# Optimization experiments

Measured on AMD Instinct MI355X. Metric: run time of the kernel, lower is better.

## Reference

```python
import jax, jax.numpy as jnp
import numpy as np

S = 10        # spiking_segment_count
TEMP = 50.0

def setup_inputs() -> dict:
    key = jax.random.key(0)
    ks = jax.random.split(key, 6)
    bs, din, dout = 2048, 1024, 1024
    x = jax.random.normal(ks[0], (bs, din), dtype=jnp.float32)
    t = jax.random.uniform(ks[1], (bs,), dtype=jnp.float32)  # in [0,1) subset of [-1,1]
    scale = 1.0 / np.sqrt(din)
    param_W = jax.random.normal(ks[2], (din, dout * S * 3), dtype=jnp.float32) * scale
    param_b = jax.random.normal(ks[3], (dout * S * 3,), dtype=jnp.float32) * 0.01
    norm_W = jax.random.normal(ks[4], (din, dout), dtype=jnp.float32) * scale
    norm_b = jax.random.normal(ks[5], (dout,), dtype=jnp.float32) * 0.01
    return {"x": x, "t": t, "param_W": param_W, "param_b": param_b,
            "norm_W": norm_W, "norm_b": norm_b}

def reference(x, t, param_W, param_b, norm_W, norm_b):
    bs = x.shape[0]
    dout = norm_W.shape[1]
    # param GEMM -> (bs, S, dout, 3)
    params = (x @ param_W + param_b).reshape(bs, S, dout, 3)
    weights = jax.nn.softmax(params[..., 0], axis=1)                 # (bs, S, dout)
    keypoints = jnp.concatenate(
        [jnp.zeros_like(weights[:, :1]), jnp.cumsum(weights, axis=1)], axis=1
    ) * 2.0 - 1.0                                                    # (bs, S+1, dout)
    slopes = jnp.tanh(params[..., 1])
    intercepts = params[..., 2]
    tt = t.reshape(-1, 1, 1)                                         # (bs, 1, 1)
    starts = keypoints[:, :S]
    ends = keypoints[:, 1:]
    residual = slopes * tt + intercepts                              # (bs, S, dout)
    validity = ((tt >= starts) & (tt < ends)) | ((tt == 1.0) & (ends == 1.0))
    vf = validity.astype(x.dtype)
    left_margin = jnp.sum((tt - starts) * vf, axis=1)                # (bs, dout)
    right_margin = jnp.sum((ends - tt) * vf, axis=1)
    lw = jax.nn.sigmoid(-TEMP * left_margin)
    rw = jax.nn.sigmoid(-TEMP * right_margin)
    lv = jnp.concatenate([vf[:, :1], vf[:, :-1]], axis=1)
    rv = jnp.concatenate([vf[:, 1:], vf[:, -1:]], axis=1)
    sw = -(lw + rw - 1.0)
    result = (lw * jnp.sum(residual * lv, axis=1)
              + sw * jnp.sum(residual * vf, axis=1)
              + rw * jnp.sum(residual * rv, axis=1))
    # norm == 'constant': subtract segment-wise integral, add norm_net(x)
    integral = jnp.sum(0.5 * slopes * (ends * ends - starts * starts)
                       + intercepts * weights, axis=1) * 0.5
    norm_target = x @ norm_W + norm_b
    return result - integral + norm_target
```

## Files before the change

kernel.cpp:

```cpp
#include <hip/hip_runtime.h>
#include <cstdint>
#include <cstddef>

#define BS    2048
#define DIN   1024
#define DOUT  1024
#define SSEG  10
#define NPAR  30720
#define NPK   20480
#define NCOL2 21504
#define NLG   10240
#define NT_LG 80
#define NT_SM 168
#define TAU   5e-5f
#define WL_CAP 1048576u

typedef _Float16 half_t;
typedef __attribute__((ext_vector_type(8))) _Float16 half8;
typedef __attribute__((ext_vector_type(4))) _Float16 half4;
typedef __attribute__((ext_vector_type(2))) _Float16 half2v;
typedef __attribute__((ext_vector_type(4))) float   floatx4;

__device__ __forceinline__ void gload16(const void* g, void* l) {
  __builtin_amdgcn_global_load_lds(
      (const __attribute__((address_space(1))) void*)g,
      (__attribute__((address_space(3))) void*)l, 16, 0, 0);
}

__global__ void k_zero(unsigned* c) { if (threadIdx.x == 0) *c = 0; }

__global__ __launch_bounds__(256) void k_split_x(const float* __restrict__ x,
                                                 half_t* __restrict__ xh,
                                                 half_t* __restrict__ xl,
                                                 unsigned* __restrict__ cnt) {
  if (blockIdx.x == 0 && threadIdx.x == 0) *cnt = 0;
  int i = blockIdx.x * 256 + threadIdx.x;
  floatx4 v = ((const floatx4*)x)[i];
  half4 h, l;
  #pragma unroll
  for (int c = 0; c < 4; c++) { h[c] = (half_t)v[c]; l[c] = (half_t)(v[c] - (float)h[c]); }
  ((half4*)xh)[i] = h;
  ((half4*)xl)[i] = l;
}

__global__ __launch_bounds__(256) void k_transw(const float* __restrict__ src,
                                                half_t* __restrict__ wsm,
                                                half_t* __restrict__ wh,
                                                half_t* __restrict__ wlo,
                                                float* __restrict__ wlt) {
  __shared__ float tile[32][384];
  int bx = blockIdx.x;
  int k0 = blockIdx.y * 32;
  int tid = threadIdx.x;
  int s  = bx >> 3;
  int d0 = (bx & 7) * 128;
  const float* sb = src + (size_t)k0 * NPAR + bx * 384;
  for (int i = tid; i < 32 * 96; i += 256) {
    int r = i / 96, q = i - r * 96;
    ((floatx4*)&tile[r][0])[q] = ((const floatx4*)(sb + (size_t)r * NPAR))[q];
  }
  __syncthreads();
  int j   = tid & 127;
  int ks  = (tid >> 7) * 16;
  {
    size_t row = (size_t)(s * 1024 + d0 + j) * DIN + k0 + ks;
    #pragma unroll
    for (int m = 0; m < 16; m++) {
      float raw = tile[ks + m][3 * j];
      float v = raw * 32.0f;
      half_t h = (half_t)v;
      wlt[row + m] = raw;
      wh [row + m] = h;
      wlo[row + m] = (half_t)(v - (float)h);
    }
  }
  #pragma unroll
  for (int c = 0; c < 2; c++) {
    size_t row = (size_t)(s * 2048 + 2 * (d0 + j) + c) * DIN + k0 + ks;
    #pragma unroll
    for (int m = 0; m < 16; m++)
      wsm[row + m] = (half_t)tile[ks + m][3 * j + 1 + c];
  }
}

__global__ __launch_bounds__(256) void k_transpose(const float* __restrict__ src,
                                                   half_t* __restrict__ dst,
                                                   int ncols, int col_off) {
  __shared__ float tile[32][33];
  int tx = threadIdx.x & 31;
  int ty = threadIdx.x >> 5;
  int col0 = blockIdx.x * 32;
  int k0   = blockIdx.y * 32;
  #pragma unroll
  for (int r = ty; r < 32; r += 8)
    tile[r][tx] = src[(size_t)(k0 + r) * ncols + col0 + tx];
  __syncthreads();
  #pragma unroll
  for (int r = ty; r < 32; r += 8)
    dst[(size_t)(col0 + r + col_off) * DIN + k0 + tx] = (half_t)tile[tx][r];
}

__global__ __launch_bounds__(256) void k_gemm_all(const half_t* __restrict__ Ah,
                                                  const half_t* __restrict__ Al,
                                                  const half_t* __restrict__ Wsm,
                                                  const half_t* __restrict__ Bh,
                                                  const half_t* __restrict__ Bl,
                                                  half_t* __restrict__ P,
                                                  float* __restrict__ Lg,
                                                  const float* __restrict__ pb,
                                                  const float* __restrict__ nb) {
  __shared__ __attribute__((aligned(16))) half_t s0[128 * 32];
  __shared__ __attribute__((aligned(16))) half_t s1[128 * 32];
  __shared__ __attribute__((aligned(16))) half_t s2[128 * 32];
  __shared__ __attribute__((aligned(16))) half_t s3[128 * 32];
  const int K = DIN;
  int bx = blockIdx.x;
  int m0 = blockIdx.y * 128;
  int tid = threadIdx.x, w = tid >> 6, L = tid & 63;
  int wm = (w >> 1) * 64, wn = (w & 1) * 64;
  int l15 = L & 15, quad = L >> 4;

  size_t arow = (size_t)(m0 + w * 16 + (L >> 2)) * K + (L & 3) * 8;
  char* l0 = (char*)s0 + w * 1024;
  char* l1 = (char*)s1 + w * 1024;
  char* l2 = (char*)s2 + w * 1024;
  char* l3 = (char*)s3 + w * 1024;

  floatx4 acc[4][4] = {};

  if (bx < NT_LG) {
    int n0 = bx * 128;
    size_t brow = (size_t)(n0 + w * 16 + (L >> 2)) * K + (L & 3) * 8;

    for (int k0 = 0; k0 < K; k0 += 32) {
      __syncthreads();
      gload16(Ah + arow + k0,          l0);
      gload16(Ah + arow + 64 * K + k0, l0 + 4096);
      gload16(Al + arow + k0,          l1);
      gload16(Al + arow + 64 * K + k0, l1 + 4096);
      gload16(Bh + brow + k0,          l2);
      gload16(Bh + brow + 64 * K + k0, l2 + 4096);
      gload16(Bl + brow + k0,          l3);
      gload16(Bl + brow + 64 * K + k0, l3 + 4096);
      __syncthreads();

      #pragma unroll
      for (int mi = 0; mi < 4; mi++) {
        half8 afh = *(const half8*)((const char*)s0 + (wm + mi * 16 + l15) * 64 + quad * 16);
        half8 afl = *(const half8*)((const char*)s1 + (wm + mi * 16 + l15) * 64 + quad * 16);
        #pragma unroll
        for (int ni = 0; ni < 4; ni++) {
          half8 bfh = *(const half8*)((const char*)s2 + (wn + ni * 16 + l15) * 64 + quad * 16);
          half8 bfl = *(const half8*)((const char*)s3 + (wn + ni * 16 + l15) * 64 + quad * 16);
          floatx4 a = acc[mi][ni];
          a = __builtin_amdgcn_mfma_f32_16x16x32_f16(afh, bfh, a, 0, 0, 0);
          a = __builtin_amdgcn_mfma_f32_16x16x32_f16(afl, bfh, a, 0, 0, 0);
          a = __builtin_amdgcn_mfma_f32_16x16x32_f16(afh, bfl, a, 0, 0, 0);
          acc[mi][ni] = a;
        }
      }
    }

    #pragma unroll
    for (int ni = 0; ni < 4; ni++) {
      int col = n0 + wn + ni * 16 + l15;
      float bias = pb[(col >> 10) * 3072 + (col & 1023) * 3];
      #pragma unroll
      for (int mi = 0; mi < 4; mi++) {
        int row = m0 + wm + mi * 16 + quad * 4;
        floatx4 v = acc[mi][ni];
        #pragma unroll
        for (int r = 0; r < 4; r++)
          Lg[(size_t)(row + r) * NLG + col] = v[r] * 0.03125f + bias;
      }
    }
  } else {
    int n0 = (bx - NT_LG) * 128;
    size_t brow = (size_t)(n0 + w * 16 + (L >> 2)) * K + (L & 3) * 8;

    for (int k0 = 0; k0 < K; k0 += 32) {
      __syncthreads();
      gload16(Ah + arow + k0,           l0);
      gload16(Ah + arow + 64 * K + k0,  l0 + 4096);
      gload16(Wsm + brow + k0,          l2);
      gload16(Wsm + brow + 64 * K + k0, l2 + 4096);
      __syncthreads();

      half8 af[4], bf[4];
      #pragma unroll
      for (int mi = 0; mi < 4; mi++)
        af[mi] = *(const half8*)((const char*)s0 + (wm + mi * 16 + l15) * 64 + quad * 16);
      #pragma unroll
      for (int ni = 0; ni < 4; ni++)
        bf[ni] = *(const half8*)((const char*)s2 + (wn + ni * 16 + l15) * 64 + quad * 16);
      #pragma unroll
      for (int mi = 0; mi < 4; mi++)
        #pragma unroll
        for (int ni = 0; ni < 4; ni++)
          acc[mi][ni] = __builtin_amdgcn_mfma_f32_16x16x32_f16(af[mi], bf[ni], acc[mi][ni], 0, 0, 0);
    }

    #pragma unroll
    for (int ni = 0; ni < 4; ni++) {
      int col = n0 + wn + ni * 16 + l15;
      float bias;
      if (col < NPK) {
        int s = col >> 11, rem = col & 2047;
        bias = pb[s * 3072 + 3 * (rem >> 1) + 1 + (rem & 1)];
      } else {
        bias = nb[col - NPK];
      }
      #pragma unroll
      for (int mi = 0; mi < 4; mi++) {
        int row = m0 + wm + mi * 16 + quad * 4;
        floatx4 v = acc[mi][ni];
        #pragma unroll
        for (int r = 0; r < 4; r++)
          P[(size_t)(row + r) * NCOL2 + col] = (half_t)(v[r] + bias);
      }
    }
  }
}

__device__ __forceinline__ float spiking_eval(const float* p, float tt, float* mind) {
  float mx = -1e30f;
  #pragma unroll
  for (int s = 0; s < SSEG; s++) mx = fmaxf(mx, p[3 * s]);
  float ew[10], wsum = 0.0f;
  #pragma unroll
  for (int s = 0; s < SSEG; s++) { ew[s] = __expf(p[3 * s] - mx); wsum += ew[s]; }
  float inv = 1.0f / wsum;

  float kp[11];
  kp[0] = -1.0f;
  float cum = 0.0f, md = 1e30f;
  #pragma unroll
  for (int s = 0; s < SSEG; s++) {
    cum += ew[s] * inv;
    kp[s + 1] = cum * 2.0f - 1.0f;
    md = fminf(md, fabsf(tt - kp[s + 1]));
  }
  *mind = md;

  float vf[10], resid[10];
  float lm = 0.0f, rm = 0.0f, integ = 0.0f;
  #pragma unroll
  for (int s = 0; s < SSEG; s++) {
    float p1 = p[3 * s + 1], p2 = p[3 * s + 2];
    float e2 = __expf(2.0f * fabsf(p1));
    float th = copysignf(1.0f - 2.0f / (e2 + 1.0f), p1);
    resid[s] = th * tt + p2;
    float st = kp[s], en = kp[s + 1];
    bool v = ((tt >= st) && (tt < en)) || ((tt == 1.0f) && (en == 1.0f));
    float vv = v ? 1.0f : 0.0f;
    vf[s] = vv;
    lm += (tt - st) * vv;
    rm += (en - tt) * vv;
    integ += 0.5f * th * (en * en - st * st) + p2 * (ew[s] * inv);
  }
  float resLV = 0.0f, resV = 0.0f, resRV = 0.0f;
  #pragma unroll
  for (int s = 0; s < SSEG; s++) {
    float lv = (s == 0) ? vf[0] : vf[s - 1];
    float rv = (s == 9) ? vf[9] : vf[s + 1];
    resLV += resid[s] * lv;
    resV  += resid[s] * vf[s];
    resRV += resid[s] * rv;
  }
  float lw = 1.0f / (1.0f + __expf(50.0f * lm));
  float rw = 1.0f / (1.0f + __expf(50.0f * rm));
  float swt = 1.0f - lw - rw;
  return lw * resLV + swt * resV + rw * resRV - 0.5f * integ + p[30];
}

__global__ __launch_bounds__(256) void k_pointwise(const half_t* __restrict__ P,
                                                   const float* __restrict__ Lg,
                                                   const float* __restrict__ t,
                                                   float* __restrict__ out,
                                                   unsigned* __restrict__ cnt,
                                                   unsigned* __restrict__ wl,
                                                   unsigned cap) {
  __shared__ __attribute__((aligned(16))) half_t sp[SSEG * 512];
  int b = blockIdx.x, dg = blockIdx.y, tid = threadIdx.x;
  const half_t* Pb = P + (size_t)b * NCOL2;
  for (int i = tid; i < SSEG * 64; i += 256) {
    int s = i >> 6, e = i & 63;
    ((uint4*)sp)[(s << 6) + e] = ((const uint4*)(Pb + s * 2048 + dg * 512))[e];
  }
  float tt = t[b];
  float nt = (float)Pb[NPK + dg * 256 + tid];
  const float* Lb = Lg + (size_t)b * NLG + dg * 256 + tid;
  __syncthreads();

  float p[31];
  #pragma unroll
  for (int s = 0; s < SSEG; s++) {
    p[3 * s] = Lb[s * 1024];
    half2v hv = ((const half2v*)sp)[s * 256 + tid];
    p[3 * s + 1] = (float)hv.x;
    p[3 * s + 2] = (float)hv.y;
  }
  p[30] = nt;
  float mind;
  float r = spiking_eval(p, tt, &mind);
  int d = dg * 256 + tid;
  out[(size_t)b * DOUT + d] = r;
  if (wl != nullptr && mind < TAU) {
    unsigned idx = atomicAdd(cnt, 1u);
    if (idx < cap) wl[idx] = ((unsigned)b << 10) | (unsigned)d;
  }
}

__global__ __launch_bounds__(256) void k_naive(const float* __restrict__ x,
                                               const float* __restrict__ t,
                                               const float* __restrict__ pW,
                                               const float* __restrict__ pb,
                                               const float* __restrict__ nW,
                                               const float* __restrict__ nb,
                                               float* __restrict__ out,
                                               unsigned* __restrict__ cnt,
                                               unsigned* __restrict__ wl,
                                               unsigned cap) {
  __shared__ float xs[DIN];
  int b = blockIdx.x, dg = blockIdx.y, tid = threadIdx.x;
  for (int i = tid; i < DIN; i += 256) xs[i] = x[(size_t)b * DIN + i];
  __syncthreads();
  int d = dg * 256 + tid;
  float acc[31];
  #pragma unroll
  for (int i = 0; i < 31; i++) acc[i] = 0.0f;
  for (int k = 0; k < DIN; k++) {
    float xv = xs[k];
    const float* wr = pW + (size_t)k * NPAR + 3 * d;
    #pragma unroll
    for (int s = 0; s < SSEG; s++) {
      acc[3 * s]     += xv * wr[s * 3072];
      acc[3 * s + 1] += xv * wr[s * 3072 + 1];
      acc[3 * s + 2] += xv * wr[s * 3072 + 2];
    }
    acc[30] += xv * nW[(size_t)k * DOUT + d];
  }
  #pragma unroll
  for (int s = 0; s < SSEG; s++) {
    acc[3 * s]     += pb[s * 3072 + 3 * d];
    acc[3 * s + 1] += pb[s * 3072 + 3 * d + 1];
    acc[3 * s + 2] += pb[s * 3072 + 3 * d + 2];
  }
  acc[30] += nb[d];
  float mind;
  float r = spiking_eval(acc, t[b], &mind);
  out[(size_t)b * DOUT + d] = r;
  if (wl != nullptr && mind < TAU) {
    unsigned idx = atomicAdd(cnt, 1u);
    if (idx < cap) wl[idx] = ((unsigned)b << 10) | (unsigned)d;
  }
}

__global__ __launch_bounds__(256) void k_redo(const float* __restrict__ x,
                                              const float* __restrict__ t,
                                              const float* __restrict__ pW,
                                              const float* __restrict__ pb,
                                              const float* __restrict__ nW,
                                              const float* __restrict__ nb,
                                              const half_t* __restrict__ P,
                                              const float* __restrict__ WLt,
                                              int haveP,
                                              const unsigned* __restrict__ cnt,
                                              const unsigned* __restrict__ wl,
                                              unsigned cap,
                                              float* __restrict__ out) {
  unsigned n = *cnt;
  if (n > cap) n = cap;
  int lane = threadIdx.x & 63;
  unsigned wave = (blockIdx.x * 256 + threadIdx.x) >> 6;
  unsigned nwaves = (gridDim.x * 256) >> 6;

  for (unsigned e = wave; e < n; e += nwaves) {
    unsigned code = wl[e];
    int b = (int)(code >> 10), d = (int)(code & 1023);

    double lg[10], sl[10], ic[10], nt = 0.0;
    #pragma unroll
    for (int s = 0; s < SSEG; s++) { lg[s] = 0.0; sl[s] = 0.0; ic[s] = 0.0; }

    if (haveP) {
      for (int k = lane; k < DIN; k += 64) {
        double xv = (double)x[(size_t)b * DIN + k];
        #pragma unroll
        for (int s = 0; s < SSEG; s++)
          lg[s] += xv * (double)WLt[(size_t)(s * 1024 + d) * DIN + k];
      }
    } else {
      for (int k = lane; k < DIN; k += 64) {
        double xv = (double)x[(size_t)b * DIN + k];
        const float* wr = pW + (size_t)k * NPAR + 3 * d;
        #pragma unroll
        for (int s = 0; s < SSEG; s++) {
          lg[s] += xv * (double)wr[s * 3072];
          sl[s] += xv * (double)wr[s * 3072 + 1];
          ic[s] += xv * (double)wr[s * 3072 + 2];
        }
        nt += xv * (double)nW[(size_t)k * DOUT + d];
      }
    }
    #pragma unroll
    for (int off = 32; off > 0; off >>= 1) {
      #pragma unroll
      for (int s = 0; s < SSEG; s++) lg[s] += __shfl_down(lg[s], off);
      if (!haveP) {
        #pragma unroll
        for (int s = 0; s < SSEG; s++) {
          sl[s] += __shfl_down(sl[s], off);
          ic[s] += __shfl_down(ic[s], off);
        }
        nt += __shfl_down(nt, off);
      }
    }

    if (lane == 0) {
      double slope[10], icpt[10], ntv;
      if (haveP) {
        const half_t* Pr = P + (size_t)b * NCOL2;
        #pragma unroll
        for (int s = 0; s < SSEG; s++) {
          slope[s] = tanh((double)(float)Pr[s * 2048 + 2 * d]);
          icpt[s]  = (double)(float)Pr[s * 2048 + 2 * d + 1];
        }
        ntv = (double)(float)Pr[NPK + d];
      } else {
        #pragma unroll
        for (int s = 0; s < SSEG; s++) {
          slope[s] = tanh(sl[s] + (double)pb[s * 3072 + 3 * d + 1]);
          icpt[s]  = ic[s] + (double)pb[s * 3072 + 3 * d + 2];
        }
        ntv = nt + (double)nb[d];
      }
      #pragma unroll
      for (int s = 0; s < SSEG; s++) lg[s] += (double)pb[s * 3072 + 3 * d];

      double mx = -1e300;
      #pragma unroll
      for (int s = 0; s < SSEG; s++) mx = fmax(mx, lg[s]);
      double ew[10], ws = 0.0;
      #pragma unroll
      for (int s = 0; s < SSEG; s++) { ew[s] = exp(lg[s] - mx); ws += ew[s]; }

      double kp[11];
      kp[0] = -1.0;
      double cum = 0.0;
      #pragma unroll
      for (int s = 0; s < SSEG; s++) { cum += ew[s] / ws; kp[s + 1] = cum * 2.0 - 1.0; }

      double tt = (double)t[b];
      double vf[10], resid[10], lm = 0.0, rm = 0.0, integ = 0.0;
      #pragma unroll
      for (int s = 0; s < SSEG; s++) {
        double st = kp[s], en = kp[s + 1];
        bool v = ((tt >= st) && (tt < en)) || ((tt == 1.0) && (en == 1.0));
        double vv = v ? 1.0 : 0.0;
        vf[s] = vv;
        resid[s] = slope[s] * tt + icpt[s];
        lm += (tt - st) * vv;
        rm += (en - tt) * vv;
        integ += 0.5 * slope[s] * (en * en - st * st) + icpt[s] * (ew[s] / ws);
      }
      double rLV = 0.0, rV = 0.0, rRV = 0.0;
      #pragma unroll
      for (int s = 0; s < SSEG; s++) {
        double lv = (s == 0) ? vf[0] : vf[s - 1];
        double rv = (s == 9) ? vf[9] : vf[s + 1];
        rLV += resid[s] * lv;
        rV  += resid[s] * vf[s];
        rRV += resid[s] * rv;
      }
      double lw = 1.0 / (1.0 + exp(50.0 * lm));
      double rw = 1.0 / (1.0 + exp(50.0 * rm));
      double res = lw * rLV + (1.0 - lw - rw) * rV + rw * rRV - 0.5 * integ + ntv;
      out[(size_t)b * DOUT + d] = (float)res;
    }
  }
}

extern "C" void kernel_launch(void* const* d_in, const int* in_sizes, int n_in,
                              void* d_out, int out_size, void* d_ws, size_t ws_size,
                              hipStream_t stream) {
  const float* x  = (const float*)d_in[0];
  const float* t  = (const float*)d_in[1];
  const float* pW = (const float*)d_in[2];
  const float* pb = (const float*)d_in[3];
  const float* nW = (const float*)d_in[4];
  const float* nb = (const float*)d_in[5];
  float* out = (float*)d_out;

  const size_t o_cnt = 0;
  const size_t o_wl  = 64;
  const size_t o_xh  = o_wl  + (size_t)WL_CAP * 4;
  const size_t o_xl  = o_xh  + (size_t)BS * DIN * 2;
  const size_t o_wsm = o_xl  + (size_t)BS * DIN * 2;
  const size_t o_wh  = o_wsm + (size_t)NCOL2 * DIN * 2;
  const size_t o_wlo = o_wh  + (size_t)NLG * DIN * 2;
  const size_t o_wlt = o_wlo + (size_t)NLG * DIN * 2;
  const size_t o_p   = o_wlt + (size_t)NLG * DIN * 4;
  const size_t o_lg  = o_p   + (size_t)BS * NCOL2 * 2;
  const size_t need  = o_lg  + (size_t)BS * NLG * 4;

  bool have_wl = ws_size >= 1024 * 1024;
  unsigned* cnt = (unsigned*)((char*)d_ws + o_cnt);
  unsigned* wl  = (unsigned*)((char*)d_ws + o_wl);
  unsigned cap  = 0;
  if (have_wl) {
    size_t avail = (ws_size >= need) ? (size_t)WL_CAP
                                     : (ws_size - o_wl) / 4;
    cap = (unsigned)(avail < WL_CAP ? avail : WL_CAP);
  }

  if (ws_size >= need) {
    half_t* xh  = (half_t*)((char*)d_ws + o_xh);
    half_t* xl  = (half_t*)((char*)d_ws + o_xl);
    half_t* wsm = (half_t*)((char*)d_ws + o_wsm);
    half_t* wh  = (half_t*)((char*)d_ws + o_wh);
    half_t* wlo = (half_t*)((char*)d_ws + o_wlo);
    float*  wlt = (float*)((char*)d_ws + o_wlt);
    half_t* P   = (half_t*)((char*)d_ws + o_p);
    float*  Lg  = (float*)((char*)d_ws + o_lg);

    k_split_x<<<(BS * DIN) / 1024, 256, 0, stream>>>(x, xh, xl, cnt);
    k_transw<<<dim3(NPAR / 384, DIN / 32), 256, 0, stream>>>(pW, wsm, wh, wlo, wlt);
    k_transpose<<<dim3(DOUT / 32, DIN / 32), 256, 0, stream>>>(nW, wsm, DOUT, NPK);
    k_gemm_all<<<dim3(NT_LG + NT_SM, BS / 128), 256, 0, stream>>>(xh, xl, wsm, wh, wlo,
                                                                  P, Lg, pb, nb);
    k_pointwise<<<dim3(BS, DOUT / 256), 256, 0, stream>>>(P, Lg, t, out, cnt,
                                                          have_wl ? wl : nullptr, cap);
    if (have_wl)
      k_redo<<<256, 256, 0, stream>>>(x, t, pW, pb, nW, nb, P, wlt, 1, cnt, wl, cap, out);
  } else {
    if (have_wl) k_zero<<<1, 64, 0, stream>>>(cnt);
    k_naive<<<dim3(BS, DOUT / 256), 256, 0, stream>>>(x, t, pW, pb, nW, nb, out, cnt,
                                                      have_wl ? wl : nullptr, cap);
    if (have_wl)
      k_redo<<<256, 256, 0, stream>>>(x, t, pW, pb, nW, nb, nullptr, nullptr, 0,
                                      cnt, wl, cap, out);
  }
}
```

Baseline: 629.9 us.

## Split fused GEMM into two kernels with swizzled tile order, merge prep kernels

Splits the combined GEMM into a 3-MFMA split-precision logit kernel and a single-precision kernel, so each kernel uses only the LDS it needs (raising occupancy for the lighter one) and avoids branch divergence across blocks. Adds a grouped block-index swizzle in which 8 consecutive blocks share one M tile and cover 8 N tiles, aimed at better L2 reuse of weight tiles. Folds the norm-weight transpose into the x-split kernel to save a launch. The cost is one extra GEMM launch and the loss of overlap between the heavy and light tile types within a single grid.

```diff
diff --git a/kernel.cpp b/kernel.cpp
--- a/kernel.cpp
+++ b/kernel.cpp
@@ -12,6 +12,7 @@
 #define NLG   10240
 #define NT_LG 80
 #define NT_SM 168
+#define MT    16
 #define TAU   5e-5f
 #define WL_CAP 1048576u
 
@@ -29,18 +30,37 @@
 
 __global__ void k_zero(unsigned* c) { if (threadIdx.x == 0) *c = 0; }
 
-__global__ __launch_bounds__(256) void k_split_x(const float* __restrict__ x,
-                                                 half_t* __restrict__ xh,
-                                                 half_t* __restrict__ xl,
-                                                 unsigned* __restrict__ cnt) {
-  if (blockIdx.x == 0 && threadIdx.x == 0) *cnt = 0;
-  int i = blockIdx.x * 256 + threadIdx.x;
-  floatx4 v = ((const floatx4*)x)[i];
-  half4 h, l;
-  #pragma unroll
-  for (int c = 0; c < 4; c++) { h[c] = (half_t)v[c]; l[c] = (half_t)(v[c] - (float)h[c]); }
-  ((half4*)xh)[i] = h;
-  ((half4*)xl)[i] = l;
+__global__ __launch_bounds__(256) void k_prep(const float* __restrict__ x,
+                                              half_t* __restrict__ xh,
+                                              half_t* __restrict__ xl,
+                                              const float* __restrict__ nW,
+                                              half_t* __restrict__ wsm,
+                                              unsigned* __restrict__ cnt) {
+  int bid = blockIdx.x;
+  if (bid < 2048) {
+    if (bid == 0 && threadIdx.x == 0) *cnt = 0;
+    int i = bid * 256 + threadIdx.x;
+    floatx4 v = ((const floatx4*)x)[i];
+    half4 h, l;
+    #pragma unroll
+    for (int c = 0; c < 4; c++) { h[c] = (half_t)v[c]; l[c] = (half_t)(v[c] - (float)h[c]); }
+    ((half4*)xh)[i] = h;
+    ((half4*)xl)[i] = l;
+  } else {
+    __shared__ float tile[32][33];
+    int b2 = bid - 2048;
+    int col0 = (b2 & 31) * 32;
+    int k0   = (b2 >> 5) * 32;
+    int tx = threadIdx.x & 31;
+    int ty = threadIdx.x >> 5;
+    #pragma unroll
+    for (int r = ty; r < 32; r += 8)
+      tile[r][tx] = nW[(size_t)(k0 + r) * DOUT + col0 + tx];
+    __syncthreads();
+    #pragma unroll
+    for (int r = ty; r < 32; r += 8)
+      wsm[(size_t)(col0 + r + NPK) * DIN + k0 + tx] = (half_t)tile[tx][r];
+  }
 }
 
 __global__ __launch_bounds__(256) void k_transw(const float* __restrict__ src,
@@ -83,141 +103,145 @@
   }
 }
 
-__global__ __launch_bounds__(256) void k_transpose(const float* __restrict__ src,
-                                                   half_t* __restrict__ dst,
-                                                   int ncols, int col_off) {
-  __shared__ float tile[32][33];
-  int tx = threadIdx.x & 31;
-  int ty = threadIdx.x >> 5;
-  int col0 = blockIdx.x * 32;
-  int k0   = blockIdx.y * 32;
-  #pragma unroll
-  for (int r = ty; r < 32; r += 8)
-    tile[r][tx] = src[(size_t)(k0 + r) * ncols + col0 + tx];
-  __syncthreads();
-  #pragma unroll
-  for (int r = ty; r < 32; r += 8)
-    dst[(size_t)(col0 + r + col_off) * DIN + k0 + tx] = (half_t)tile[tx][r];
-}
-
-__global__ __launch_bounds__(256) void k_gemm_all(const half_t* __restrict__ Ah,
-                                                  const half_t* __restrict__ Al,
-                                                  const half_t* __restrict__ Wsm,
-                                                  const half_t* __restrict__ Bh,
-                                                  const half_t* __restrict__ Bl,
-                                                  half_t* __restrict__ P,
-                                                  float* __restrict__ Lg,
-                                                  const float* __restrict__ pb,
-                                                  const float* __restrict__ nb) {
-  __shared__ __attribute__((aligned(16))) half_t s0[128 * 32];
-  __shared__ __attribute__((aligned(16))) half_t s1[128 * 32];
-  __shared__ __attribute__((aligned(16))) half_t s2[128 * 32];
-  __shared__ __attribute__((aligned(16))) half_t s3[128 * 32];
+__device__ __forceinline__ void swizzle_mn(int bid, int* mt, int* nt) {
+  int x = bid & 7;
+  int g = bid >> 3;
+  *mt = g & 15;
+  *nt = (g >> 4) * 8 + x;
+}
+
+__global__ __launch_bounds__(256) void k_gemm_logit(const half_t* __restrict__ Ah,
+                                                    const half_t* __restrict__ Al,
+                                                    const half_t* __restrict__ Bh,
+                                                    const half_t* __restrict__ Bl,
+                                                    float* __restrict__ Lg,
+                                                    const float* __restrict__ pb) {
+  __shared__ __attribute__((aligned(16))) half_t sAh[128 * 32];
+  __shared__ __attribute__((aligned(16))) half_t sAl[128 * 32];
+  __shared__ __attribute__((aligned(16))) half_t sBh[128 * 32];
+  __shared__ __attribute__((aligned(16))) half_t sBl[128 * 32];
   const int K = DIN;
-  int bx = blockIdx.x;
-  int m0 = blockIdx.y * 128;
+  int mt, nt;
+  swizzle_mn(blockIdx.x, &mt, &nt);
+  int m0 = mt * 128, n0 = nt * 128;
   int tid = threadIdx.x, w = tid >> 6, L = tid & 63;
   int wm = (w >> 1) * 64, wn = (w & 1) * 64;
   int l15 = L & 15, quad = L >> 4;
 
   size_t arow = (size_t)(m0 + w * 16 + (L >> 2)) * K + (L & 3) * 8;
-  char* l0 = (char*)s0 + w * 1024;
-  char* l1 = (char*)s1 + w * 1024;
-  char* l2 = (char*)s2 + w * 1024;
-  char* l3 = (char*)s3 + w * 1024;
+  size_t brow = (size_t)(n0 + w * 16 + (L >> 2)) * K + (L & 3) * 8;
+  char* lah = (char*)sAh + w * 1024;
+  char* lal = (char*)sAl + w * 1024;
+  char* lbh = (char*)sBh + w * 1024;
+  char* lbl = (char*)sBl + w * 1024;
 
   floatx4 acc[4][4] = {};
 
-  if (bx < NT_LG) {
-    int n0 = bx * 128;
-    size_t brow = (size_t)(n0 + w * 16 + (L >> 2)) * K + (L & 3) * 8;
-
-    for (int k0 = 0; k0 < K; k0 += 32) {
-      __syncthreads();
-      gload16(Ah + arow + k0,          l0);
-      gload16(Ah + arow + 64 * K + k0, l0 + 4096);
-      gload16(Al + arow + k0,          l1);
-      gload16(Al + arow + 64 * K + k0, l1 + 4096);
-      gload16(Bh + brow + k0,          l2);
-      gload16(Bh + brow + 64 * K + k0, l2 + 4096);
-      gload16(Bl + brow + k0,          l3);
-      gload16(Bl + brow + 64 * K + k0, l3 + 4096);
-      __syncthreads();
-
-      #pragma unroll
-      for (int mi = 0; mi < 4; mi++) {
-        half8 afh = *(const half8*)((const char*)s0 + (wm + mi * 16 + l15) * 64 + quad * 16);
-        half8 afl = *(const half8*)((const char*)s1 + (wm + mi * 16 + l15) * 64 + quad * 16);
-        #pragma unroll
-        for (int ni = 0; ni < 4; ni++) {
-          half8 bfh = *(const half8*)((const char*)s2 + (wn + ni * 16 + l15) * 64 + quad * 16);
-          half8 bfl = *(const half8*)((const char*)s3 + (wn + ni * 16 + l15) * 64 + quad * 16);
-          floatx4 a = acc[mi][ni];
-          a = __builtin_amdgcn_mfma_f32_16x16x32_f16(afh, bfh, a, 0, 0, 0);
-          a = __builtin_amdgcn_mfma_f32_16x16x32_f16(afl, bfh, a, 0, 0, 0);
-          a = __builtin_amdgcn_mfma_f32_16x16x32_f16(afh, bfl, a, 0, 0, 0);
-          acc[mi][ni] = a;
-        }
-      }
-    }
-
-    #pragma unroll
-    for (int ni = 0; ni < 4; ni++) {
-      int col = n0 + wn + ni * 16 + l15;
-      float bias = pb[(col >> 10) * 3072 + (col & 1023) * 3];
-      #pragma unroll
-      for (int mi = 0; mi < 4; mi++) {
-        int row = m0 + wm + mi * 16 + quad * 4;
-        floatx4 v = acc[mi][ni];
-        #pragma unroll
-        for (int r = 0; r < 4; r++)
-          Lg[(size_t)(row + r) * NLG + col] = v[r] * 0.03125f + bias;
-      }
-    }
-  } else {
-    int n0 = (bx - NT_LG) * 128;
-    size_t brow = (size_t)(n0 + w * 16 + (L >> 2)) * K + (L & 3) * 8;
-
-    for (int k0 = 0; k0 < K; k0 += 32) {
-      __syncthreads();
-      gload16(Ah + arow + k0,           l0);
-      gload16(Ah + arow + 64 * K + k0,  l0 + 4096);
-      gload16(Wsm + brow + k0,          l2);
-      gload16(Wsm + brow + 64 * K + k0, l2 + 4096);
-      __syncthreads();
-
-      half8 af[4], bf[4];
-      #pragma unroll
-      for (int mi = 0; mi < 4; mi++)
-        af[mi] = *(const half8*)((const char*)s0 + (wm + mi * 16 + l15) * 64 + quad * 16);
+  for (int k0 = 0; k0 < K; k0 += 32) {
+    __syncthreads();
+    gload16(Ah + arow + k0,          lah);
+    gload16(Ah + arow + 64 * K + k0, lah + 4096);
+    gload16(Al + arow + k0,          lal);
+    gload16(Al + arow + 64 * K + k0, lal + 4096);
+    gload16(Bh + brow + k0,          lbh);
+    gload16(Bh + brow + 64 * K + k0, lbh + 4096);
+    gload16(Bl + brow + k0,          lbl);
+    gload16(Bl + brow + 64 * K + k0, lbl + 4096);
+    __syncthreads();
+
+    #pragma unroll
+    for (int mi = 0; mi < 4; mi++) {
+      half8 afh = *(const half8*)((const char*)sAh + (wm + mi * 16 + l15) * 64 + quad * 16);
+      half8 afl = *(const half8*)((const char*)sAl + (wm + mi * 16 + l15) * 64 + quad * 16);
+      #pragma unroll
+      for (int ni = 0; ni < 4; ni++) {
+        half8 bfh = *(const half8*)((const char*)sBh + (wn + ni * 16 + l15) * 64 + quad * 16);
+        half8 bfl = *(const half8*)((const char*)sBl + (wn + ni * 16 + l15) * 64 + quad * 16);
+        floatx4 a = acc[mi][ni];
+        a = __builtin_amdgcn_mfma_f32_16x16x32_f16(afh, bfh, a, 0, 0, 0);
+        a = __builtin_amdgcn_mfma_f32_16x16x32_f16(afl, bfh, a, 0, 0, 0);
+        a = __builtin_amdgcn_mfma_f32_16x16x32_f16(afh, bfl, a, 0, 0, 0);
+        acc[mi][ni] = a;
+      }
+    }
+  }
+
+  #pragma unroll
+  for (int ni = 0; ni < 4; ni++) {
+    int col = n0 + wn + ni * 16 + l15;
+    float bias = pb[(col >> 10) * 3072 + (col & 1023) * 3];
+    #pragma unroll
+    for (int mi = 0; mi < 4; mi++) {
+      int row = m0 + wm + mi * 16 + quad * 4;
+      floatx4 v = acc[mi][ni];
+      #pragma unroll
+      for (int r = 0; r < 4; r++)
+        Lg[(size_t)(row + r) * NLG + col] = v[r] * 0.03125f + bias;
+    }
+  }
+}
+
+__global__ __launch_bounds__(256) void k_gemm_sm(const half_t* __restrict__ A,
+                                                 const half_t* __restrict__ B,
+                                                 half_t* __restrict__ P,
+                                                 const float* __restrict__ pb,
+                                                 const float* __restrict__ nb) {
+  __shared__ __attribute__((aligned(16))) half_t As[128 * 32];
+  __shared__ __attribute__((aligned(16))) half_t Bs[128 * 32];
+  const int K = DIN;
+  int mt, nt;
+  swizzle_mn(blockIdx.x, &mt, &nt);
+  int m0 = mt * 128, n0 = nt * 128;
+  int tid = threadIdx.x, w = tid >> 6, L = tid & 63;
+  int wm = (w >> 1) * 64, wn = (w & 1) * 64;
+  int l15 = L & 15, quad = L >> 4;
+
+  const half_t* ga = A + (size_t)(m0 + w * 16 + (L >> 2)) * K + (L & 3) * 8;
+  const half_t* gb = B + (size_t)(n0 + w * 16 + (L >> 2)) * K + (L & 3) * 8;
+  char* lA = (char*)As + w * 1024;
+  char* lB = (char*)Bs + w * 1024;
+
+  floatx4 acc[4][4] = {};
+
+  for (int k0 = 0; k0 < K; k0 += 32) {
+    __syncthreads();
+    gload16(ga + k0,          lA);
+    gload16(ga + 64 * K + k0, lA + 4096);
+    gload16(gb + k0,          lB);
+    gload16(gb + 64 * K + k0, lB + 4096);
+    __syncthreads();
+
+    half8 af[4], bf[4];
+    #pragma unroll
+    for (int mi = 0; mi < 4; mi++)
+      af[mi] = *(const half8*)((const char*)As + (wm + mi * 16 + l15) * 64 + quad * 16);
+    #pragma unroll
+    for (int ni = 0; ni < 4; ni++)
+      bf[ni] = *(const half8*)((const char*)Bs + (wn + ni * 16 + l15) * 64 + quad * 16);
+    #pragma unroll
+    for (int mi = 0; mi < 4; mi++)
       #pragma unroll
       for (int ni = 0; ni < 4; ni++)
-        bf[ni] = *(const half8*)((const char*)s2 + (wn + ni * 16 + l15) * 64 + quad * 16);
-      #pragma unroll
-      for (int mi = 0; mi < 4; mi++)
-        #pragma unroll
-        for (int ni = 0; ni < 4; ni++)
-          acc[mi][ni] = __builtin_amdgcn_mfma_f32_16x16x32_f16(af[mi], bf[ni], acc[mi][ni], 0, 0, 0);
-    }
-
-    #pragma unroll
-    for (int ni = 0; ni < 4; ni++) {
-      int col = n0 + wn + ni * 16 + l15;
-      float bias;
-      if (col < NPK) {
-        int s = col >> 11, rem = col & 2047;
-        bias = pb[s * 3072 + 3 * (rem >> 1) + 1 + (rem & 1)];
-      } else {
-        bias = nb[col - NPK];
-      }
-      #pragma unroll
-      for (int mi = 0; mi < 4; mi++) {
-        int row = m0 + wm + mi * 16 + quad * 4;
-        floatx4 v = acc[mi][ni];
-        #pragma unroll
-        for (int r = 0; r < 4; r++)
-          P[(size_t)(row + r) * NCOL2 + col] = (half_t)(v[r] + bias);
-      }
+        acc[mi][ni] = __builtin_amdgcn_mfma_f32_16x16x32_f16(af[mi], bf[ni], acc[mi][ni], 0, 0, 0);
+  }
+
+  #pragma unroll
+  for (int ni = 0; ni < 4; ni++) {
+    int col = n0 + wn + ni * 16 + l15;
+    float bias;
+    if (col < NPK) {
+      int s = col >> 11, rem = col & 2047;
+      bias = pb[s * 3072 + 3 * (rem >> 1) + 1 + (rem & 1)];
+    } else {
+      bias = nb[col - NPK];
+    }
+    #pragma unroll
+    for (int mi = 0; mi < 4; mi++) {
+      int row = m0 + wm + mi * 16 + quad * 4;
+      floatx4 v = acc[mi][ni];
+      #pragma unroll
+      for (int r = 0; r < 4; r++)
+        P[(size_t)(row + r) * NCOL2 + col] = (half_t)(v[r] + bias);
     }
   }
 }
@@ -524,11 +548,10 @@
     half_t* P   = (half_t*)((char*)d_ws + o_p);
     float*  Lg  = (float*)((char*)d_ws + o_lg);
 
-    k_split_x<<<(BS * DIN) / 1024, 256, 0, stream>>>(x, xh, xl, cnt);
+    k_prep<<<3072, 256, 0, stream>>>(x, xh, xl, nW, wsm, cnt);
     k_transw<<<dim3(NPAR / 384, DIN / 32), 256, 0, stream>>>(pW, wsm, wh, wlo, wlt);
-    k_transpose<<<dim3(DOUT / 32, DIN / 32), 256, 0, stream>>>(nW, wsm, DOUT, NPK);
-    k_gemm_all<<<dim3(NT_LG + NT_SM, BS / 128), 256, 0, stream>>>(xh, xl, wsm, wh, wlo,
-                                                                  P, Lg, pb, nb);
+    k_gemm_logit<<<NT_LG * MT, 256, 0, stream>>>(xh, xl, wh, wlo, Lg, pb);
+    k_gemm_sm<<<NT_SM * MT, 256, 0, stream>>>(xh, wsm, P, pb, nb);
     k_pointwise<<<dim3(BS, DOUT / 256), 256, 0, stream>>>(P, Lg, t, out, cnt,
                                                           have_wl ? wl : nullptr, cap);
     if (have_wl)
```

After: 618.2 us. Within noise of the previous version (-1.9%).
